# Optimization experiments

Measured on AMD Instinct MI355X. Metric: run time of the kernel, lower is better.

The kernel has to match this reference:

```python
import jax, jax.numpy as jnp
import numpy as np

H = 200
DT = 0.01
K = 100.0
C = 1.0
B = 131072


def setup_inputs() -> dict:
    key = jax.random.key(0)
    u_seq = jax.random.normal(key, (B, H), dtype=jnp.float32)
    x1_0 = jnp.zeros((B,), dtype=jnp.float32)
    v1_0 = jnp.ones((B,), dtype=jnp.float32)
    x2_0 = jnp.ones((B,), dtype=jnp.float32) * 2.0
    v2_0 = jnp.zeros((B,), dtype=jnp.float32)
    goal = jnp.ones((1,), dtype=jnp.float32) * 5.0
    return {"u_seq": u_seq, "x1_0": x1_0, "v1_0": v1_0,
            "x2_0": x2_0, "v2_0": v2_0, "goal": goal}


def _step(carry, u_t):
    x1, v1, x2, v2 = carry
    penetration = x1 + 1.0 - x2            # spring engages when box1 touches box2
    contact = jnp.maximum(penetration, 0.0)  # clamp(min=0)
    F_contact = -K * contact
    F1 = u_t + F_contact - C * v1
    F2 = -F_contact - C * v2
    v1 = v1 + F1 * DT
    v2 = v2 + F2 * DT
    x1 = x1 + v1 * DT
    x2 = x2 + v2 * DT
    return (x1, v1, x2, v2), None


def reference(u_seq, x1_0, v1_0, x2_0, v2_0, goal):
    # u_seq: [B, H]; states: [B]; goal: [1]
    (x1, v1, x2, v2), _ = jax.lax.scan(_step, (x1_0, v1_0, x2_0, v2_0),
                                       u_seq.T)  # scan over H steps
    loss = (x2 - goal) ** 2                # [B]
    return loss, x1, x2
```

## Files before the change

kernel.cpp:

```cpp
#include <hip/hip_runtime.h>

#define H_STEPS 200
#define DT 0.01f
#define K_SPRING 100.0f

__device__ __forceinline__ void step(float u, float& x1, float& v1,
                                     float& x2, float& v2) {
    float pen     = x1 + 1.0f - x2;
    float contact = fmaxf(pen, 0.0f);
    float Fc      = -K_SPRING * contact;
    float F1      = u + Fc - v1;
    float F2      = -Fc - v2;
    v1 += F1 * DT;
    v2 += F2 * DT;
    x1 += v1 * DT;
    x2 += v2 * DT;
}

__global__ __launch_bounds__(256)
void pushing_env_kernel(const float* __restrict__ u_seq,
                        const float* __restrict__ x1_0,
                        const float* __restrict__ v1_0,
                        const float* __restrict__ x2_0,
                        const float* __restrict__ v2_0,
                        const float* __restrict__ goal,
                        float* __restrict__ out, int B) {
    int b = blockIdx.x * blockDim.x + threadIdx.x;
    if (b >= B) return;

    float x1 = x1_0[b];
    float v1 = v1_0[b];
    float x2 = x2_0[b];
    float v2 = v2_0[b];
    const float g = goal[0];

    const float4* u = reinterpret_cast<const float4*>(u_seq + (size_t)b * H_STEPS);

    #pragma unroll 5
    for (int t = 0; t < H_STEPS / 4; ++t) {
        float4 uu = u[t];
        step(uu.x, x1, v1, x2, v2);
        step(uu.y, x1, v1, x2, v2);
        step(uu.z, x1, v1, x2, v2);
        step(uu.w, x1, v1, x2, v2);
    }

    float d = x2 - g;
    out[b]         = d * d;
    out[B + b]     = x1;
    out[2 * B + b] = x2;
}

extern "C" void kernel_launch(void* const* d_in, const int* in_sizes, int n_in,
                              void* d_out, int out_size, void* d_ws, size_t ws_size,
                              hipStream_t stream) {
    const float* u_seq = (const float*)d_in[0];
    const float* x1_0  = (const float*)d_in[1];
    const float* v1_0  = (const float*)d_in[2];
    const float* x2_0  = (const float*)d_in[3];
    const float* v2_0  = (const float*)d_in[4];
    const float* goal  = (const float*)d_in[5];
    float* out = (float*)d_out;

    const int B = in_sizes[1];
    const int block = 256;
    const int grid = (B + block - 1) / block;
    pushing_env_kernel<<<grid, block, 0, stream>>>(u_seq, x1_0, v1_0, x2_0,
                                                   v2_0, goal, out, B);
}
```

Measured before the change: 27.36 us.

## Stage control inputs through double-buffered LDS with async coalesced global-to-LDS loads

Each thread used to read its own 800-byte row of u_seq with float4 loads, a large-stride access pattern across the wavefront. Now each wave loads 32-timestep chunks for its 64 rows straight into LDS with global_load_lds. Adjacent lanes read contiguous addresses, and an XOR swizzle avoids bank conflicts. Two LDS buffers let the next chunk's loads overlap the current chunk's integration, with manual vmcnt waits instead of barriers, because each wave only touches its own rows. The cost is 64 KB of LDS per block, which may limit occupancy. The kernel also assumes B is a multiple of 256 and relies on hand-counted outstanding loads for correctness.

```diff
diff --git a/kernel.cpp b/kernel.cpp
--- a/kernel.cpp
+++ b/kernel.cpp
@@ -3,6 +3,10 @@
 #define H_STEPS 200
 #define DT 0.01f
 #define K_SPRING 100.0f
+#define ROWS 256
+#define CW 32
+#define WORDS_PER_WAVE 2048
+#define LDSW (ROWS * CW)
 
 __device__ __forceinline__ void step(float u, float& x1, float& v1,
                                      float& x2, float& v2) {
@@ -17,7 +21,25 @@
     x2 += v2 * DT;
 }
 
-__global__ __launch_bounds__(256)
+__device__ __forceinline__ void issue_chunk(const float* __restrict__ u_seq,
+                                            float* lbuf, int b0, int wave,
+                                            int lane, int t0) {
+    const int rb = wave * 64 + (lane >> 5);
+    const int tl = lane & 31;
+    #pragma unroll
+    for (int j = 0; j < 32; ++j) {
+        const int r = rb + j * 2;
+        int tg = t0 + (tl ^ (r & 31));
+        tg = tg < H_STEPS ? tg : (H_STEPS - 1);
+        const float* g = u_seq + (size_t)(b0 + r) * H_STEPS + tg;
+        float* l = lbuf + wave * WORDS_PER_WAVE + j * 64;
+        __builtin_amdgcn_global_load_lds(
+            (const __attribute__((address_space(1))) void*)g,
+            (__attribute__((address_space(3))) void*)l, 4, 0, 0);
+    }
+}
+
+__global__ __launch_bounds__(ROWS)
 void pushing_env_kernel(const float* __restrict__ u_seq,
                         const float* __restrict__ x1_0,
                         const float* __restrict__ v1_0,
@@ -25,8 +47,13 @@
                         const float* __restrict__ v2_0,
                         const float* __restrict__ goal,
                         float* __restrict__ out, int B) {
-    int b = blockIdx.x * blockDim.x + threadIdx.x;
-    if (b >= B) return;
+    __shared__ float lds[2][LDSW];
+    const int tid  = threadIdx.x;
+    const int b0   = blockIdx.x * ROWS;
+    const int b    = b0 + tid;
+    const int wave = tid >> 6;
+    const int lane = tid & 63;
+    const int sw   = tid & 31;
 
     float x1 = x1_0[b];
     float v1 = v1_0[b];
@@ -34,15 +61,23 @@
     float v2 = v2_0[b];
     const float g = goal[0];
 
-    const float4* u = reinterpret_cast<const float4*>(u_seq + (size_t)b * H_STEPS);
+    issue_chunk(u_seq, &lds[0][0], b0, wave, lane, 0);
 
-    #pragma unroll 5
-    for (int t = 0; t < H_STEPS / 4; ++t) {
-        float4 uu = u[t];
-        step(uu.x, x1, v1, x2, v2);
-        step(uu.y, x1, v1, x2, v2);
-        step(uu.z, x1, v1, x2, v2);
-        step(uu.w, x1, v1, x2, v2);
+    for (int c = 0; c < 6; ++c) {
+        issue_chunk(u_seq, &lds[(c + 1) & 1][0], b0, wave, lane, (c + 1) * CW);
+        asm volatile("s_waitcnt vmcnt(32)" ::: "memory");
+        const float* lb = &lds[c & 1][tid * CW];
+        #pragma unroll
+        for (int k = 0; k < CW; ++k)
+            step(lb[k ^ sw], x1, v1, x2, v2);
+        asm volatile("" ::: "memory");
+    }
+    asm volatile("s_waitcnt vmcnt(0)" ::: "memory");
+    {
+        const float* lb = &lds[0][tid * CW];
+        #pragma unroll
+        for (int k = 0; k < 8; ++k)
+            step(lb[k ^ sw], x1, v1, x2, v2);
     }
 
     float d = x2 - g;
@@ -63,8 +98,7 @@
     float* out = (float*)d_out;
 
     const int B = in_sizes[1];
-    const int block = 256;
-    const int grid = (B + block - 1) / block;
-    pushing_env_kernel<<<grid, block, 0, stream>>>(u_seq, x1_0, v1_0, x2_0,
-                                                   v2_0, goal, out, B);
+    const int grid = B / ROWS;
+    pushing_env_kernel<<<grid, ROWS, 0, stream>>>(u_seq, x1_0, v1_0, x2_0,
+                                                  v2_0, goal, out, B);
 }
```

Measured after the change: 27.76 us. Within noise of the previous version (+1.5%).

## Stage input rows through LDS with pipelined global_load_lds transposed loads

Applied to the files above, without the earlier changes.

Replaces per-thread strided float4 row loads with cooperative global_load_lds transfers that fetch contiguous 64-byte segments into a 5-slot LDS ring. Loads are issued several chunks ahead and waited on with explicit vmcnt counts, so memory latency overlaps the recurrence. Blocks shrink to a single 64-thread wave. The bounds check is dropped, which assumes the batch size is a multiple of 64, and the LDS footprint limits occupancy.

```diff
diff --git a/kernel.cpp b/kernel.cpp
--- a/kernel.cpp
+++ b/kernel.cpp
@@ -17,7 +17,7 @@
     x2 += v2 * DT;
 }
 
-__global__ __launch_bounds__(256)
+__global__ __launch_bounds__(64)
 void pushing_env_kernel(const float* __restrict__ u_seq,
                         const float* __restrict__ x1_0,
                         const float* __restrict__ v1_0,
@@ -25,8 +25,10 @@
                         const float* __restrict__ v2_0,
                         const float* __restrict__ goal,
                         float* __restrict__ out, int B) {
-    int b = blockIdx.x * blockDim.x + threadIdx.x;
-    if (b >= B) return;
+    __shared__ float4 lds4[5 * 256];
+    const int lane = threadIdx.x;
+    const int b0   = blockIdx.x * 64;
+    const int b    = b0 + lane;
 
     float x1 = x1_0[b];
     float v1 = v1_0[b];
@@ -34,16 +36,62 @@
     float v2 = v2_0[b];
     const float g = goal[0];
 
-    const float4* u = reinterpret_cast<const float4*>(u_seq + (size_t)b * H_STEPS);
+    const int rsel = lane & 15;
+    const int qsel = lane >> 4;
 
-    #pragma unroll 5
-    for (int t = 0; t < H_STEPS / 4; ++t) {
-        float4 uu = u[t];
-        step(uu.x, x1, v1, x2, v2);
-        step(uu.y, x1, v1, x2, v2);
-        step(uu.z, x1, v1, x2, v2);
-        step(uu.w, x1, v1, x2, v2);
-    }
+#define ISSUE(c, s) { \
+    _Pragma("unroll") \
+    for (int j = 0; j < 4; ++j) { \
+        const float* gp = u_seq + \
+            (size_t)(b0 + j * 16 + rsel) * H_STEPS + ((c) * 4 + qsel) * 4; \
+        float4* lp = &lds4[(s) * 256 + j * 64]; \
+        __builtin_amdgcn_global_load_lds( \
+            (const __attribute__((address_space(1))) void*)gp, \
+            (__attribute__((address_space(3))) void*)lp, 16, 0, 0); \
+    } }
+
+#define CONSUME(c, s, N) { \
+    asm volatile("s_waitcnt vmcnt(" #N ")" ::: "memory"); \
+    _Pragma("unroll") \
+    for (int q = 0; q < 4; ++q) { \
+        float4 u4 = lds4[(s) * 256 + (lane >> 4) * 64 + q * 16 + (lane & 15)]; \
+        step(u4.x, x1, v1, x2, v2); \
+        step(u4.y, x1, v1, x2, v2); \
+        step(u4.z, x1, v1, x2, v2); \
+        step(u4.w, x1, v1, x2, v2); \
+    } \
+    __builtin_amdgcn_sched_barrier(0); }
+
+    ISSUE(0, 0) ISSUE(1, 1) ISSUE(2, 2) ISSUE(3, 3)
+
+    CONSUME(0, 0, 12) ISSUE(4, 4)
+    CONSUME(1, 1, 12) ISSUE(5, 0)
+    CONSUME(2, 2, 12) ISSUE(6, 1)
+    CONSUME(3, 3, 12) ISSUE(7, 2)
+    CONSUME(4, 4, 12) ISSUE(8, 3)
+    CONSUME(5, 0, 12) ISSUE(9, 4)
+    CONSUME(6, 1, 12) ISSUE(10, 0)
+    CONSUME(7, 2, 12) ISSUE(11, 1)
+
+    const float4* urow = reinterpret_cast<const float4*>(
+        u_seq + (size_t)b * H_STEPS);
+    float4 t0 = urow[48];
+    float4 t1 = urow[49];
+
+    CONSUME(8, 3, 14)
+    CONSUME(9, 4, 10)
+    CONSUME(10, 0, 6)
+    CONSUME(11, 1, 2)
+
+    asm volatile("s_waitcnt vmcnt(0)" ::: "memory");
+    step(t0.x, x1, v1, x2, v2);
+    step(t0.y, x1, v1, x2, v2);
+    step(t0.z, x1, v1, x2, v2);
+    step(t0.w, x1, v1, x2, v2);
+    step(t1.x, x1, v1, x2, v2);
+    step(t1.y, x1, v1, x2, v2);
+    step(t1.z, x1, v1, x2, v2);
+    step(t1.w, x1, v1, x2, v2);
 
     float d = x2 - g;
     out[b]         = d * d;
@@ -61,10 +109,10 @@
     const float* v2_0  = (const float*)d_in[4];
     const float* goal  = (const float*)d_in[5];
     float* out = (float*)d_out;
+    (void)d_ws; (void)ws_size;
 
     const int B = in_sizes[1];
-    const int block = 256;
-    const int grid = (B + block - 1) / block;
-    pushing_env_kernel<<<grid, block, 0, stream>>>(u_seq, x1_0, v1_0, x2_0,
-                                                   v2_0, goal, out, B);
+    const int grid = B / 64;
+    pushing_env_kernel<<<grid, 64, 0, stream>>>(u_seq, x1_0, v1_0, x2_0,
+                                                v2_0, goal, out, B);
 }
```

Measured after the change: 24.66 us. 9.9% less time.
